# Optimization experiments

Measured on AMD Instinct MI355X. Metric: run time of the kernel, lower is better.

The kernel has to match this reference:

```python
import jax, jax.numpy as jnp
import numpy as np

B, H, S, D = 8, 12, 1024, 64

def setup_inputs() -> dict:
    key = jax.random.key(0)
    kq, kk, kv = jax.random.split(key, 3)
    q = jax.random.normal(kq, (B, H, S, D), dtype=jnp.float32)
    k = jax.random.normal(kk, (B, H, S, D), dtype=jnp.float32)
    v = jax.random.normal(kv, (B, H, S, D), dtype=jnp.float32)
    scale = 8  # sqrt(d_head)
    return {"q": q, "k": k, "v": v, "scale": scale}

def reference(q, k, v, scale):
    # scores: (B,H,S,S) = q @ k^T / scale, softmax over last axis
    scores = jnp.einsum('bhqd,bhkd->bhqk', q, k) / scale
    attention_score = jax.nn.softmax(scores, axis=-1)
    # context: (B,H,S,D)
    attention_context = jnp.einsum('bhqk,bhkd->bhqd', attention_score, v)
    return (attention_score, attention_context)
```

## Files before the change

kernel.cpp:

```cpp
#include <hip/hip_runtime.h>


#define SLEN 1024
#define DHEAD 64
#define NBH 96

typedef __attribute__((ext_vector_type(4))) float f32x4;
typedef __attribute__((ext_vector_type(8))) __bf16 bf16x8;

#define PL_STRIDE 1032
#define VT_STRIDE 72

struct SMem {
  __bf16 pl[64][PL_STRIDE];
  union {
    __bf16 qt[64][VT_STRIDE];
    __bf16 vt[64][VT_STRIDE];
  } u;
  float red[8][64];
  float mrow[64];
  float invrow[64];
};

__global__ __launch_bounds__(512, 2)
void attn_fused(const float* __restrict__ Qp, const float* __restrict__ Kp,
                const float* __restrict__ Vp, const int* __restrict__ scale_p,
                float* __restrict__ out) {
  __shared__ SMem sm;
  const int tid  = threadIdx.x;
  const int w    = tid >> 6;
  const int lane = tid & 63;
  const int quad = lane >> 4;
  const int c16  = lane & 15;
  const int bh   = blockIdx.y;
  const int qbase = blockIdx.x * 64;

  int siv = *scale_p;
  float fs = (siv >= 1 && siv <= (1 << 24)) ? (float)siv : __int_as_float(siv);
  const float inv_scale = 1.0f / fs;

  const float* Qg = Qp + ((size_t)bh * SLEN + qbase) * DHEAD;
  const float* Kg = Kp + (size_t)bh * SLEN * DHEAD;
  const float* Vg = Vp + (size_t)bh * SLEN * DHEAD;

  #pragma unroll
  for (int it = 0; it < 2; ++it) {
    int flat = it * 2048 + tid * 4;
    int r = flat >> 6, d = flat & 63;
    f32x4 qv = *(const f32x4*)(Qg + (size_t)r * DHEAD + d);
    #pragma unroll
    for (int j = 0; j < 4; ++j)
      sm.u.qt[r][d + j] = (__bf16)(qv[j] * inv_scale);
  }
  __syncthreads();

  bf16x8 af[4][2];
  #pragma unroll
  for (int rt = 0; rt < 4; ++rt)
    #pragma unroll
    for (int k0 = 0; k0 < 2; ++k0)
      af[rt][k0] = *(const bf16x8*)&sm.u.qt[rt * 16 + c16][k0 * 32 + quad * 8];

  f32x4 acc[4][8];
  {
    f32x4 z = {0.0f, 0.0f, 0.0f, 0.0f};
    #pragma unroll
    for (int rt = 0; rt < 4; ++rt)
      #pragma unroll
      for (int ct = 0; ct < 8; ++ct) acc[rt][ct] = z;
  }

  #pragma unroll
  for (int ct = 0; ct < 8; ++ct) {
    int krow = w * 128 + ct * 16 + c16;
    const float* kr = Kg + (size_t)krow * DHEAD + quad * 8;
    f32x4 k0a = *(const f32x4*)(kr);
    f32x4 k0b = *(const f32x4*)(kr + 4);
    f32x4 k1a = *(const f32x4*)(kr + 32);
    f32x4 k1b = *(const f32x4*)(kr + 36);
    bf16x8 b0, b1;
    #pragma unroll
    for (int j = 0; j < 4; ++j) {
      b0[j]     = (__bf16)k0a[j];
      b0[j + 4] = (__bf16)k0b[j];
      b1[j]     = (__bf16)k1a[j];
      b1[j + 4] = (__bf16)k1b[j];
    }
    #pragma unroll
    for (int rt = 0; rt < 4; ++rt) {
      acc[rt][ct] = __builtin_amdgcn_mfma_f32_16x16x32_bf16(af[rt][0], b0, acc[rt][ct], 0, 0, 0);
      acc[rt][ct] = __builtin_amdgcn_mfma_f32_16x16x32_bf16(af[rt][1], b1, acc[rt][ct], 0, 0, 0);
    }
  }

  float mx[4][4];
  #pragma unroll
  for (int rt = 0; rt < 4; ++rt)
    #pragma unroll
    for (int i = 0; i < 4; ++i) {
      float m = acc[rt][0][i];
      #pragma unroll
      for (int ct = 1; ct < 8; ++ct) m = fmaxf(m, acc[rt][ct][i]);
      mx[rt][i] = m;
    }
  #pragma unroll
  for (int off = 1; off < 16; off <<= 1)
    #pragma unroll
    for (int rt = 0; rt < 4; ++rt)
      #pragma unroll
      for (int i = 0; i < 4; ++i)
        mx[rt][i] = fmaxf(mx[rt][i], __shfl_xor(mx[rt][i], off));
  if (c16 == 0) {
    #pragma unroll
    for (int rt = 0; rt < 4; ++rt)
      #pragma unroll
      for (int i = 0; i < 4; ++i)
        sm.red[w][rt * 16 + quad * 4 + i] = mx[rt][i];
  }
  __syncthreads();
  if (tid < 64) {
    float m = sm.red[0][tid];
    #pragma unroll
    for (int w2 = 1; w2 < 8; ++w2) m = fmaxf(m, sm.red[w2][tid]);
    sm.mrow[tid] = m;
  }
  __syncthreads();

  float sum4[4][4];
  #pragma unroll
  for (int rt = 0; rt < 4; ++rt)
    #pragma unroll
    for (int i = 0; i < 4; ++i) {
      float m = sm.mrow[rt * 16 + quad * 4 + i];
      float s = 0.0f;
      #pragma unroll
      for (int ct = 0; ct < 8; ++ct) {
        float e = __expf(acc[rt][ct][i] - m);
        acc[rt][ct][i] = e;
        s += e;
      }
      sum4[rt][i] = s;
    }
  #pragma unroll
  for (int off = 1; off < 16; off <<= 1)
    #pragma unroll
    for (int rt = 0; rt < 4; ++rt)
      #pragma unroll
      for (int i = 0; i < 4; ++i)
        sum4[rt][i] += __shfl_xor(sum4[rt][i], off);
  if (c16 == 0) {
    #pragma unroll
    for (int rt = 0; rt < 4; ++rt)
      #pragma unroll
      for (int i = 0; i < 4; ++i)
        sm.red[w][rt * 16 + quad * 4 + i] = sum4[rt][i];
  }
  __syncthreads();
  if (tid < 64) {
    float s = 0.0f;
    #pragma unroll
    for (int w2 = 0; w2 < 8; ++w2) s += sm.red[w2][tid];
    sm.invrow[tid] = 1.0f / s;
  }
  __syncthreads();

  #pragma unroll
  for (int rt = 0; rt < 4; ++rt) {
    #pragma unroll
    for (int i = 0; i < 4; ++i) {
      int row = rt * 16 + quad * 4 + i;
      float inv = sm.invrow[row];
      float* orow = out + ((size_t)bh * SLEN + qbase + row) * SLEN;
      __bf16* prow = sm.pl[row];
      #pragma unroll
      for (int ct = 0; ct < 8; ++ct) {
        int col = w * 128 + ct * 16 + c16;
        float p = acc[rt][ct][i] * inv;
        orow[col] = p;
        prow[col] = (__bf16)p;
      }
    }
  }

  f32x4 ctx[2];
  {
    f32x4 z = {0.0f, 0.0f, 0.0f, 0.0f};
    ctx[0] = z; ctx[1] = z;
  }
  const int prt = w & 3;
  const int dtb = w >> 2;

  f32x4 pref[2];
  #pragma unroll
  for (int it = 0; it < 2; ++it) {
    int flat = it * 2048 + tid * 4;
    int kk = flat >> 6, d0 = flat & 63;
    pref[it] = *(const f32x4*)(Vg + (size_t)kk * DHEAD + d0);
  }

  for (int kc = 0; kc < 16; ++kc) {
    __syncthreads();
    #pragma unroll
    for (int it = 0; it < 2; ++it) {
      int flat = it * 2048 + tid * 4;
      int kk = flat >> 6, d0 = flat & 63;
      #pragma unroll
      for (int j = 0; j < 4; ++j)
        sm.u.vt[d0 + j][kk] = (__bf16)pref[it][j];
    }
    if (kc < 15) {
      #pragma unroll
      for (int it = 0; it < 2; ++it) {
        int flat = it * 2048 + tid * 4;
        int kk = flat >> 6, d0 = flat & 63;
        pref[it] = *(const f32x4*)(Vg + (size_t)((kc + 1) * 64 + kk) * DHEAD + d0);
      }
    }
    __syncthreads();
    #pragma unroll
    for (int ks = 0; ks < 2; ++ks) {
      int kl = ks * 32 + quad * 8;
      bf16x8 a = *(const bf16x8*)&sm.pl[prt * 16 + c16][kc * 64 + kl];
      #pragma unroll
      for (int t2 = 0; t2 < 2; ++t2) {
        int dt = dtb + t2 * 2;
        bf16x8 b = *(const bf16x8*)&sm.u.vt[dt * 16 + c16][kl];
        ctx[t2] = __builtin_amdgcn_mfma_f32_16x16x32_bf16(a, b, ctx[t2], 0, 0, 0);
      }
    }
  }

  float* outC = out + (size_t)NBH * SLEN * SLEN;
  #pragma unroll
  for (int t2 = 0; t2 < 2; ++t2) {
    int dt = dtb + t2 * 2;
    #pragma unroll
    for (int i = 0; i < 4; ++i) {
      int row = prt * 16 + quad * 4 + i;
      outC[((size_t)bh * SLEN + qbase + row) * DHEAD + dt * 16 + c16] = ctx[t2][i];
    }
  }
}

extern "C" void kernel_launch(void* const* d_in, const int* in_sizes, int n_in,
                              void* d_out, int out_size, void* d_ws, size_t ws_size,
                              hipStream_t stream) {
  (void)in_sizes; (void)n_in; (void)d_ws; (void)ws_size; (void)out_size;
  const float* q = (const float*)d_in[0];
  const float* k = (const float*)d_in[1];
  const float* v = (const float*)d_in[2];
  const int* scale = (const int*)d_in[3];
  float* out = (float*)d_out;
  dim3 grid(SLEN / 64, NBH);
  dim3 block(512);
  hipLaunchKernelGGL(attn_fused, grid, block, 0, stream, q, k, v, scale, out);
}
```

Baseline: 633.4 us.

## Permute P/V shared layout for vector stores, widen V chunks, nontemporal output stores

Stores each lane's eight bf16 probabilities as one 16-byte vector into shared memory, using a permuted key-column order, and transposes V into a matching permuted column order so the PV MFMA reduction stays consistent. V is staged in 128-key chunks (8 iterations instead of 16), and its first prefetch is issued before the score write-out. Output stores for the attention matrix and context use nontemporal hints to limit cache pollution. The goal is fewer LDS store instructions, fewer barriers, and better overlap of the large probability write with V loads. The cost is a larger V tile in shared memory and a layout permutation that has to match exactly for results to stay correct.

Measured after the change: 645.9 us. Within noise of the previous version (+2.0%).

```diff
diff --git a/kernel.cpp b/kernel.cpp
--- a/kernel.cpp
+++ b/kernel.cpp
@@ -9,12 +9,13 @@
 typedef __attribute__((ext_vector_type(8))) __bf16 bf16x8;
 
 #define PL_STRIDE 1032
-#define VT_STRIDE 72
+#define QT_STRIDE 72
+#define VT_STRIDE 136
 
 struct SMem {
   __bf16 pl[64][PL_STRIDE];
   union {
-    __bf16 qt[64][VT_STRIDE];
+    __bf16 qt[64][QT_STRIDE];
     __bf16 vt[64][VT_STRIDE];
   } u;
   float red[8][64];
@@ -164,6 +165,16 @@
   }
   __syncthreads();
 
+  const int kap = tid & 127;
+  const int dgb = tid >> 7;
+  const int scol = (kap & 15) * 8 + (kap >> 4);
+  f32x4 pref[4];
+  #pragma unroll
+  for (int it = 0; it < 4; ++it) {
+    int d0 = it * 16 + dgb * 4;
+    pref[it] = *(const f32x4*)(Vg + (size_t)kap * DHEAD + d0);
+  }
+
   #pragma unroll
   for (int rt = 0; rt < 4; ++rt) {
     #pragma unroll
@@ -171,14 +182,14 @@
       int row = rt * 16 + quad * 4 + i;
       float inv = sm.invrow[row];
       float* orow = out + ((size_t)bh * SLEN + qbase + row) * SLEN;
-      __bf16* prow = sm.pl[row];
+      bf16x8 pk;
       #pragma unroll
       for (int ct = 0; ct < 8; ++ct) {
-        int col = w * 128 + ct * 16 + c16;
         float p = acc[rt][ct][i] * inv;
-        orow[col] = p;
-        prow[col] = (__bf16)p;
-      }
+        __builtin_nontemporal_store(p, &orow[w * 128 + ct * 16 + c16]);
+        pk[ct] = (__bf16)p;
+      }
+      *(bf16x8*)&sm.pl[row][w * 128 + c16 * 8] = pk;
     }
   }
 
@@ -190,41 +201,30 @@
   const int prt = w & 3;
   const int dtb = w >> 2;
 
-  f32x4 pref[2];
-  #pragma unroll
-  for (int it = 0; it < 2; ++it) {
-    int flat = it * 2048 + tid * 4;
-    int kk = flat >> 6, d0 = flat & 63;
-    pref[it] = *(const f32x4*)(Vg + (size_t)kk * DHEAD + d0);
-  }
-
-  for (int kc = 0; kc < 16; ++kc) {
+  for (int sp = 0; sp < 8; ++sp) {
     __syncthreads();
     #pragma unroll
-    for (int it = 0; it < 2; ++it) {
-      int flat = it * 2048 + tid * 4;
-      int kk = flat >> 6, d0 = flat & 63;
+    for (int it = 0; it < 4; ++it) {
+      int d0 = it * 16 + dgb * 4;
       #pragma unroll
       for (int j = 0; j < 4; ++j)
-        sm.u.vt[d0 + j][kk] = (__bf16)pref[it][j];
-    }
-    if (kc < 15) {
-      #pragma unroll
-      for (int it = 0; it < 2; ++it) {
-        int flat = it * 2048 + tid * 4;
-        int kk = flat >> 6, d0 = flat & 63;
-        pref[it] = *(const f32x4*)(Vg + (size_t)((kc + 1) * 64 + kk) * DHEAD + d0);
-      }
+        sm.u.vt[d0 + j][scol] = (__bf16)pref[it][j];
     }
     __syncthreads();
-    #pragma unroll
-    for (int ks = 0; ks < 2; ++ks) {
-      int kl = ks * 32 + quad * 8;
-      bf16x8 a = *(const bf16x8*)&sm.pl[prt * 16 + c16][kc * 64 + kl];
+    if (sp < 7) {
+      #pragma unroll
+      for (int it = 0; it < 4; ++it) {
+        int d0 = it * 16 + dgb * 4;
+        pref[it] = *(const f32x4*)(Vg + (size_t)((sp + 1) * 128 + kap) * DHEAD + d0);
+      }
+    }
+    #pragma unroll
+    for (int b2 = 0; b2 < 4; ++b2) {
+      bf16x8 a = *(const bf16x8*)&sm.pl[prt * 16 + c16][sp * 128 + b2 * 32 + quad * 8];
       #pragma unroll
       for (int t2 = 0; t2 < 2; ++t2) {
         int dt = dtb + t2 * 2;
-        bf16x8 b = *(const bf16x8*)&sm.u.vt[dt * 16 + c16][kl];
+        bf16x8 b = *(const bf16x8*)&sm.u.vt[dt * 16 + c16][b2 * 32 + quad * 8];
         ctx[t2] = __builtin_amdgcn_mfma_f32_16x16x32_bf16(a, b, ctx[t2], 0, 0, 0);
       }
     }
@@ -237,7 +237,9 @@
     #pragma unroll
     for (int i = 0; i < 4; ++i) {
       int row = prt * 16 + quad * 4 + i;
-      outC[((size_t)bh * SLEN + qbase + row) * DHEAD + dt * 16 + c16] = ctx[t2][i];
+      __builtin_nontemporal_store(
+          ctx[t2][i],
+          &outC[((size_t)bh * SLEN + qbase + row) * DHEAD + dt * 16 + c16]);
     }
   }
 }
```
